# Performance work log

Measured on AMD Instinct MI355X. Metric: run time of the kernel, lower is better.

The kernel has to match this reference:

```python
import jax, jax.numpy as jnp
import numpy as np

NUM_GROUPS = 4
EPS = 1e-6


def group_norm(x, scale, bias):
    # x: [b, c, h, w]; GroupNorm32 computes stats in fp32 (x already fp32 here)
    b, c, h, w = x.shape
    xg = x.reshape(b, NUM_GROUPS, c // NUM_GROUPS, h, w)
    mean = jnp.mean(xg, axis=(2, 3, 4), keepdims=True)
    var = jnp.var(xg, axis=(2, 3, 4), keepdims=True)
    xn = ((xg - mean) * jax.lax.rsqrt(var + EPS)).reshape(b, c, h, w)
    return xn * scale[None, :, None, None] + bias[None, :, None, None]


def conv1x1(x, w, b):
    # 1x1 conv == channel mix: x [b,c,h,w], w [co,ci]
    return jnp.einsum('bchw,dc->bdhw', x, w) + b[None, :, None, None]


def setup_inputs() -> dict:
    key = jax.random.key(0)
    ks = jax.random.split(key, 6)
    c = 256
    s = 1.0 / np.sqrt(c)
    return {
        'x': jax.random.normal(ks[0], (4, c, 64, 64), dtype=jnp.float32),
        'gn_scale': jnp.ones((c,), jnp.float32),
        'gn_bias': jnp.zeros((c,), jnp.float32),
        'wq': jax.random.normal(ks[1], (c, c), jnp.float32) * s,
        'bq': jnp.zeros((c,), jnp.float32),
        'wk': jax.random.normal(ks[2], (c, c), jnp.float32) * s,
        'bk': jnp.zeros((c,), jnp.float32),
        'wv': jax.random.normal(ks[3], (c, c), jnp.float32) * s,
        'bv': jnp.zeros((c,), jnp.float32),
        'wproj': jax.random.normal(ks[4], (c, c), jnp.float32) * s,
        'bproj': jnp.zeros((c,), jnp.float32),
    }


def reference(x, gn_scale, gn_bias, wq, bq, wk, bk, wv, bv, wproj, bproj):
    b, c, h, w = x.shape
    hw = h * w
    h_ = group_norm(x, gn_scale, gn_bias)
    q = conv1x1(h_, wq, bq).reshape(b, c, hw)  # [b, c, hw]
    k = conv1x1(h_, wk, bk).reshape(b, c, hw)
    v = conv1x1(h_, wv, bv).reshape(b, c, hw)
    scale = jnp.float32(1.0 / np.sqrt(c))
    # attn[b, i, j] = sum_c q[b,c,i] * k[b,c,j], fp32 softmax over j
    attn = jnp.einsum('bci,bcj->bij', q.astype(jnp.float32), k.astype(jnp.float32)) * scale
    attn = jax.nn.softmax(attn, axis=-1).astype(x.dtype)
    # out[b, c, i] = sum_j v[b,c,j] * attn[b,i,j]
    out = jnp.einsum('bcj,bij->bci', v, attn).reshape(b, c, h, w)
    out = conv1x1(out, wproj, bproj)
    return x + out
```

## Files before the change

kernel.cpp:

```cpp
#include <hip/hip_runtime.h>


#define HW 4096
#define CCH 256
#define NBATCH 4
#define GN_N (64 * HW)

typedef unsigned short u16;
typedef __attribute__((ext_vector_type(8))) short bf16x8;
typedef __attribute__((ext_vector_type(4))) float f32x4;
typedef __attribute__((ext_vector_type(4))) u16 u16x4;

__device__ __forceinline__ u16 f2bf(float f) {
  unsigned u = __float_as_uint(f);
  u += 0x7fffu + ((u >> 16) & 1u);
  return (u16)(u >> 16);
}
__device__ __forceinline__ float bf2f(u16 h) { return __uint_as_float(((unsigned)h) << 16); }

__device__ __forceinline__ void gload_lds16(const void* g, void* l) {
  __builtin_amdgcn_global_load_lds(
      (const __attribute__((address_space(1))) unsigned*)g,
      (__attribute__((address_space(3))) unsigned*)l, 16, 0, 0);
}

__global__ __launch_bounds__(256) void gn_partial(const float* __restrict__ x,
                                                  float* __restrict__ part) {
  const int bg = blockIdx.y, blk = blockIdx.x, tid = threadIdx.x;
  const float4* X = (const float4*)(x + (size_t)bg * GN_N);
  float s = 0.f, ss = 0.f;
#pragma unroll
  for (int u = 0; u < 8; ++u) {
    float4 v = X[blk * 2048 + u * 256 + tid];
    s += v.x + v.y + v.z + v.w;
    ss += v.x * v.x + v.y * v.y + v.z * v.z + v.w * v.w;
  }
  for (int off = 32; off; off >>= 1) { s += __shfl_xor(s, off); ss += __shfl_xor(ss, off); }
  __shared__ float rs[4], rss[4];
  const int w = tid >> 6;
  if ((tid & 63) == 0) { rs[w] = s; rss[w] = ss; }
  __syncthreads();
  if (tid == 0) {
    part[(bg * 32 + blk) * 2 + 0] = rs[0] + rs[1] + rs[2] + rs[3];
    part[(bg * 32 + blk) * 2 + 1] = rss[0] + rss[1] + rss[2] + rss[3];
  }
}

__global__ void gn_finalize(const float* __restrict__ part, float2* __restrict__ stats) {
  const int t = threadIdx.x;
  if (t < 16) {
    float s = 0.f, ss = 0.f;
    for (int u = 0; u < 32; ++u) { s += part[(t * 32 + u) * 2]; ss += part[(t * 32 + u) * 2 + 1]; }
    const float mean = s * (1.0f / GN_N);
    const float var = ss * (1.0f / GN_N) - mean * mean;
    stats[t] = make_float2(mean, rsqrtf(var + 1e-6f));
  }
}

__global__ __launch_bounds__(256) void norm_tr(const float* __restrict__ x,
                                               const float2* __restrict__ stats,
                                               const float* __restrict__ gsc,
                                               const float* __restrict__ gbi,
                                               u16* __restrict__ Ht) {
  __shared__ u16 T[64][72];
  const int i0 = blockIdx.x * 64, c0 = blockIdx.y * 64, b = blockIdx.z;
  const int tid = threadIdx.x;
  const int cl = tid >> 4;
  const int il4 = (tid & 15) * 4;
#pragma unroll
  for (int it = 0; it < 4; ++it) {
    const int c = c0 + it * 16 + cl;
    const float2 st = stats[b * 4 + (c >> 6)];
    const float sc = gsc[c] * st.y;
    const float bi = gbi[c] - st.x * sc;
    const float4 v = *(const float4*)&x[((size_t)(b * CCH + c)) * HW + i0 + il4];
    T[il4 + 0][it * 16 + cl] = f2bf(v.x * sc + bi);
    T[il4 + 1][it * 16 + cl] = f2bf(v.y * sc + bi);
    T[il4 + 2][it * 16 + cl] = f2bf(v.z * sc + bi);
    T[il4 + 3][it * 16 + cl] = f2bf(v.w * sc + bi);
  }
  __syncthreads();
  const int il = tid >> 2, cs = (tid & 3) * 16;
  const uint4 a = *(const uint4*)&T[il][cs];
  const uint4 b2 = *(const uint4*)&T[il][cs + 8];
  const size_t o = ((size_t)b * HW + i0 + il) * CCH + c0 + cs;
  *(uint4*)&Ht[o] = a;
  *(uint4*)&Ht[o + 8] = b2;
}

__global__ __launch_bounds__(256) void wcast(const float* __restrict__ w0, const float* __restrict__ w1,
                                             const float* __restrict__ w2, const float* __restrict__ w3,
                                             u16* __restrict__ dst) {
  const float* src = blockIdx.y == 0 ? w0 : blockIdx.y == 1 ? w1 : blockIdx.y == 2 ? w2 : w3;
  u16* d = dst + (size_t)blockIdx.y * 65536;
  const int idx = (blockIdx.x * 256 + threadIdx.x) * 8;
  const float4 a = *(const float4*)&src[idx];
  const float4 c = *(const float4*)&src[idx + 4];
  uint4 p;
  p.x = (unsigned)f2bf(a.x) | ((unsigned)f2bf(a.y) << 16);
  p.y = (unsigned)f2bf(a.z) | ((unsigned)f2bf(a.w) << 16);
  p.z = (unsigned)f2bf(c.x) | ((unsigned)f2bf(c.y) << 16);
  p.w = (unsigned)f2bf(c.z) | ((unsigned)f2bf(c.w) << 16);
  *(uint4*)&d[idx] = p;
}

template <int EPI, bool HASB>
__global__ __launch_bounds__(256) void gemm2(
    const u16* __restrict__ A, int lda, long sA,
    const u16* __restrict__ Bm, int ldb, long sB,
    void* __restrict__ O0, int ldo, long sO,
    void* __restrict__ O1, void* __restrict__ O2,
    const float* __restrict__ b0, const float* __restrict__ b1, const float* __restrict__ b2,
    const float* __restrict__ aux, long sAux,
    float scale, int K) {
  __shared__ char lsA[32768], lsB[32768];
  int bx, by, bz;
  {
    const int nx = gridDim.x, ny = gridDim.y;
    const int lin = blockIdx.x + nx * (blockIdx.y + ny * blockIdx.z);
    const int q = (nx * ny * (int)gridDim.z) >> 3;
    const int wg = (lin & 7) * q + (lin >> 3);
    bx = wg % nx; const int t2 = wg / nx; by = t2 % ny; bz = t2 / ny;
  }
  const int tid = threadIdx.x;
  const int w = tid >> 6, l = tid & 63;
  const int wm = w >> 1, wn = w & 1;
  const int m0 = by * 128, n0 = bx * 128;
  const u16* Ab = A + (size_t)bz * sA;
  const u16* Bb = Bm + (size_t)bz * sB;

  f32x4 acc[4][4];
#pragma unroll
  for (int i = 0; i < 4; ++i)
#pragma unroll
    for (int j = 0; j < 4; ++j)
#pragma unroll
      for (int q2 = 0; q2 < 4; ++q2) acc[i][j][q2] = 0.f;

  auto stage = [&](int buf, int k0) {
#pragma unroll
    for (int s = 0; s < 4; ++s) {
      const int o = s * 4096 + tid * 16;
      const int r = o >> 7;
      const int c = ((o >> 4) & 7) ^ (r & 7);
      const int ke = c * 8;
      gload_lds16(Ab + (size_t)(m0 + r) * lda + k0 + ke, lsA + buf * 16384 + s * 4096 + w * 1024);
      gload_lds16(Bb + (size_t)(n0 + r) * ldb + k0 + ke, lsB + buf * 16384 + s * 4096 + w * 1024);
    }
  };

  const int nt = K >> 6;
  stage(0, 0);
  asm volatile("s_waitcnt vmcnt(0)" ::: "memory");
  __syncthreads();
  for (int t = 0; t < nt; ++t) {
    const int cur = t & 1;
    if (t + 1 < nt) stage(cur ^ 1, (t + 1) << 6);
#pragma unroll
    for (int kk = 0; kk < 2; ++kk) {
      bf16x8 aF[4], bF[4];
#pragma unroll
      for (int mi = 0; mi < 4; ++mi) {
        const int r = wm * 64 + mi * 16 + (l & 15);
        const int cc = (kk * 4 + (l >> 4)) ^ (r & 7);
        aF[mi] = *(const bf16x8*)(lsA + cur * 16384 + r * 128 + cc * 16);
      }
#pragma unroll
      for (int ni = 0; ni < 4; ++ni) {
        const int r = wn * 64 + ni * 16 + (l & 15);
        const int cc = (kk * 4 + (l >> 4)) ^ (r & 7);
        bF[ni] = *(const bf16x8*)(lsB + cur * 16384 + r * 128 + cc * 16);
      }
#pragma unroll
      for (int mi = 0; mi < 4; ++mi)
#pragma unroll
        for (int ni = 0; ni < 4; ++ni)
          acc[mi][ni] = __builtin_amdgcn_mfma_f32_16x16x32_bf16(aF[mi], bF[ni], acc[mi][ni], 0, 0, 0);
    }
    asm volatile("s_waitcnt vmcnt(0)" ::: "memory");
    __syncthreads();
  }

  const int lc = l & 15;
  const int lr4 = (l >> 4) * 4;

  if (EPI == 5) {
    const int sel = m0 >> 8;
    const float* bs = sel == 0 ? b0 : sel == 1 ? b1 : b2;
#pragma unroll
    for (int mi = 0; mi < 4; ++mi) {
      const int mg = m0 + wm * 64 + mi * 16 + lr4;
      const int mloc = mg & 255;
      const float4 bv = *(const float4*)&bs[mloc];
      float bb4[4] = {bv.x, bv.y, bv.z, bv.w};
#pragma unroll
      for (int ni = 0; ni < 4; ++ni) {
        const int n = n0 + wn * 64 + ni * 16 + lc;
        if (sel == 2) {
          u16* V = (u16*)O2 + (size_t)bz * sO;
#pragma unroll
          for (int q2 = 0; q2 < 4; ++q2) V[(size_t)(mloc + q2) * HW + n] = f2bf(acc[mi][ni][q2] + bb4[q2]);
        } else {
          u16* Oq = (u16*)(sel == 0 ? O0 : O1) + (size_t)bz * sO;
          u16x4 pk;
#pragma unroll
          for (int q2 = 0; q2 < 4; ++q2) pk[q2] = f2bf(acc[mi][ni][q2] + bb4[q2]);
          *(u16x4*)&Oq[(size_t)n * CCH + mloc] = pk;
        }
      }
    }
  } else {
    float* O = (float*)O0 + (size_t)bz * sO;
    const float* R = aux + (size_t)bz * sAux;
#pragma unroll
    for (int mi = 0; mi < 4; ++mi) {
      const int mb = m0 + wm * 64 + mi * 16 + lr4;
      float bb4[4] = {0.f, 0.f, 0.f, 0.f};
      if (HASB) {
        const float4 bv = *(const float4*)&b0[mb];
        bb4[0] = bv.x; bb4[1] = bv.y; bb4[2] = bv.z; bb4[3] = bv.w;
      }
#pragma unroll
      for (int ni = 0; ni < 4; ++ni) {
        const int n = n0 + wn * 64 + ni * 16 + lc;
#pragma unroll
        for (int q2 = 0; q2 < 4; ++q2)
          O[(size_t)(mb + q2) * ldo + n] = acc[mi][ni][q2] * scale + bb4[q2] + R[(size_t)(mb + q2) * ldo + n];
      }
    }
  }
}

#define LBUFA 32768
__global__ __launch_bounds__(256) void attn_fused(
    const u16* __restrict__ Qt, const u16* __restrict__ Kt, const u16* __restrict__ Vv,
    float* __restrict__ Opart, float* __restrict__ Rpart) {
  __shared__ __attribute__((aligned(16))) char lds[2 * LBUFA];
  __shared__ __attribute__((aligned(16))) unsigned P_block[64][20];
  const int bid = blockIdx.x;
  const int it = bid >> 3, b = (bid >> 1) & 3, jh = bid & 1;
  const int tid = threadIdx.x, w = tid >> 6, l = tid & 63;
  const int g = l >> 4, base = l & 15;
  const u16* Qb = Qt + (size_t)b * HW * CCH;
  const u16* Kb = Kt + (size_t)b * HW * CCH;
  const u16* Vb = Vv + (size_t)b * CCH * HW;
  const int iw0 = it * 64 + w * 16;

  bf16x8 q[8];
#pragma unroll
  for (int kc = 0; kc < 8; ++kc)
    q[kc] = *(const bf16x8*)&Qb[(size_t)(iw0 + base) * CCH + kc * 32 + g * 8];

  f32x4 oacc[4][4];
#pragma unroll
  for (int fi = 0; fi < 4; ++fi)
#pragma unroll
    for (int cf = 0; cf < 4; ++cf)
#pragma unroll
      for (int r = 0; r < 4; ++r) oacc[fi][cf][r] = 0.f;
  float rsum = 0.f;

  auto stage = [&](int buf, int j0) {
    char* Kl = lds + buf * LBUFA;
    char* Vl = Kl + 16384;
#pragma unroll
    for (int s = 0; s < 8; ++s) {
      const int i = s * 4 + w;
      if (i < 16) {
        const int row = i * 2 + (l >> 5);
        const int c5 = l & 31;
        gload_lds16(Kb + (size_t)(j0 + row) * CCH + ((c5 ^ (row & 7)) * 8), Kl + i * 1024);
      } else {
        const int jj = i - 16;
        const int jg = jj >> 2, sub = jj & 3;
        const int cc = sub * 64 + l;
        gload_lds16(Vb + (size_t)cc * HW + j0 + jg * 8, Vl + jg * 4096 + sub * 1024);
      }
    }
  };

  const int j0base = jh * 2048;
  const int NT = 64;
  stage(0, j0base);
  asm volatile("s_waitcnt vmcnt(0)" ::: "memory");
  __builtin_amdgcn_s_barrier();

  for (int t = 0; t < NT; ++t) {
    const int cur = t & 1;
    if (t + 1 < NT) stage(cur ^ 1, j0base + (t + 1) * 32);
    const char* Kl = lds + cur * LBUFA;
    const char* Vl = Kl + 16384;
    f32x4 sacc[2];
#pragma unroll
    for (int mj = 0; mj < 2; ++mj)
#pragma unroll
      for (int r = 0; r < 4; ++r) sacc[mj][r] = 0.f;
    __builtin_amdgcn_s_setprio(1);
#pragma unroll
    for (int kc = 0; kc < 8; ++kc) {
      bf16x8 kf[2];
#pragma unroll
      for (int mj = 0; mj < 2; ++mj) {
        const int row = mj * 16 + base;
        const int c5 = (kc * 4 + g) ^ (row & 7);
        kf[mj] = *(const bf16x8*)(Kl + row * 512 + c5 * 16);
      }
#pragma unroll
      for (int mj = 0; mj < 2; ++mj)
        sacc[mj] = __builtin_amdgcn_mfma_f32_16x16x32_bf16(kf[mj], q[kc], sacc[mj], 0, 0, 0);
    }
    __builtin_amdgcn_s_setprio(0);
    const int iL = w * 16 + base;
#pragma unroll
    for (int mj = 0; mj < 2; ++mj) {
      const float p0 = __expf(sacc[mj][0] * 0.0625f - 8.0f);
      const float p1 = __expf(sacc[mj][1] * 0.0625f - 8.0f);
      const float p2 = __expf(sacc[mj][2] * 0.0625f - 8.0f);
      const float p3 = __expf(sacc[mj][3] * 0.0625f - 8.0f);
      const u16 e0 = f2bf(p0), e1 = f2bf(p1), e2 = f2bf(p2), e3 = f2bf(p3);
      rsum += (bf2f(e0) + bf2f(e1)) + (bf2f(e2) + bf2f(e3));
      P_block[iL][mj * 8 + g * 2 + 0] = (unsigned)e0 | ((unsigned)e1 << 16);
      P_block[iL][mj * 8 + g * 2 + 1] = (unsigned)e2 | ((unsigned)e3 << 16);
    }
    asm volatile("s_waitcnt lgkmcnt(0)" ::: "memory");
    __builtin_amdgcn_sched_barrier(0);
    __builtin_amdgcn_s_barrier();
    bf16x8 vf[4];
#pragma unroll
    for (int cf = 0; cf < 4; ++cf)
      vf[cf] = *(const bf16x8*)(Vl + g * 4096 + (w * 64 + cf * 16 + base) * 16);
    __builtin_amdgcn_s_setprio(1);
#pragma unroll
    for (int fi = 0; fi < 4; ++fi) {
      const bf16x8 af = *(const bf16x8*)&P_block[fi * 16 + base][g * 4];
#pragma unroll
      for (int cf = 0; cf < 4; ++cf)
        oacc[fi][cf] = __builtin_amdgcn_mfma_f32_16x16x32_bf16(af, vf[cf], oacc[fi][cf], 0, 0, 0);
    }
    __builtin_amdgcn_s_setprio(0);
    asm volatile("s_waitcnt vmcnt(0) lgkmcnt(0)" ::: "memory");
    __builtin_amdgcn_sched_barrier(0);
    __builtin_amdgcn_s_barrier();
  }

  rsum += __shfl_xor(rsum, 16);
  rsum += __shfl_xor(rsum, 32);
  if (l < 16) Rpart[(size_t)jh * 16384 + b * HW + iw0 + l] = rsum;
  float* Op = Opart + (size_t)jh * 16384 * CCH + (size_t)b * HW * CCH + (size_t)it * 64 * CCH;
#pragma unroll
  for (int fi = 0; fi < 4; ++fi) {
#pragma unroll
    for (int cf = 0; cf < 4; ++cf) {
      const int c = w * 64 + cf * 16 + base;
#pragma unroll
      for (int r = 0; r < 4; ++r)
        Op[(size_t)(fi * 16 + g * 4 + r) * CCH + c] = oacc[fi][cf][r];
    }
  }
}

__global__ __launch_bounds__(256) void attn_combine(const float* __restrict__ Op,
                                                    const float* __restrict__ Rp,
                                                    u16* __restrict__ Ot) {
  const int idx = blockIdx.x * 256 + threadIdx.x;
  const int row = idx >> 6;
  const int c4 = (idx & 63) * 4;
  const float4 o0 = *(const float4*)&Op[(size_t)row * CCH + c4];
  const float4 o1 = *(const float4*)&Op[(size_t)16384 * CCH + (size_t)row * CCH + c4];
  const float inv = 1.0f / (Rp[row] + Rp[16384 + row]);
  u16x4 r;
  r[0] = f2bf((o0.x + o1.x) * inv);
  r[1] = f2bf((o0.y + o1.y) * inv);
  r[2] = f2bf((o0.z + o1.z) * inv);
  r[3] = f2bf((o0.w + o1.w) * inv);
  *(u16x4*)&Ot[(size_t)row * CCH + c4] = r;
}

extern "C" void kernel_launch(void* const* d_in, const int* in_sizes, int n_in,
                              void* d_out, int out_size, void* d_ws, size_t ws_size,
                              hipStream_t stream) {
  const float* x   = (const float*)d_in[0];
  const float* gsc = (const float*)d_in[1];
  const float* gbi = (const float*)d_in[2];
  const float* wq  = (const float*)d_in[3];
  const float* bq  = (const float*)d_in[4];
  const float* wk  = (const float*)d_in[5];
  const float* bk  = (const float*)d_in[6];
  const float* wv  = (const float*)d_in[7];
  const float* bv  = (const float*)d_in[8];
  const float* wp  = (const float*)d_in[9];
  const float* bp  = (const float*)d_in[10];
  float* out = (float*)d_out;

  char* ws = (char*)d_ws;
  size_t off = 0;
  auto alloc = [&](size_t bytes) {
    size_t o = off; off = (off + bytes + 255) & ~(size_t)255; return o;
  };
  const size_t szMat = (size_t)NBATCH * HW * CCH * 2;
  u16* W      = (u16*)(ws + alloc(4 * 65536 * 2));
  float* pgn  = (float*)(ws + alloc(16 * 32 * 2 * 4));
  float2* st  = (float2*)(ws + alloc(16 * 8));
  u16* Ht = (u16*)(ws + alloc(szMat));
  u16* Qt = (u16*)(ws + alloc(szMat));
  u16* Kt = (u16*)(ws + alloc(szMat));
  u16* Vv = (u16*)(ws + alloc(szMat));
  u16* Ot = (u16*)(ws + alloc(szMat));
  float* Opart = (float*)(ws + alloc((size_t)2 * 16384 * CCH * 4));
  float* Rpart = (float*)(ws + alloc((size_t)2 * 16384 * 4));

  const long sM = (long)HW * CCH;

  wcast<<<dim3(32, 4), 256, 0, stream>>>(wq, wk, wv, wp, W);
  gn_partial<<<dim3(32, 16), 256, 0, stream>>>(x, pgn);
  gn_finalize<<<1, 64, 0, stream>>>(pgn, st);
  norm_tr<<<dim3(HW / 64, CCH / 64, NBATCH), 256, 0, stream>>>(x, st, gsc, gbi, Ht);

  gemm2<5, true><<<dim3(32, 6, NBATCH), 256, 0, stream>>>(
      W, 256, 0, Ht, 256, sM, Qt, 256, sM, Kt, Vv, bq, bk, bv, nullptr, 0, 1.f, 256);

  attn_fused<<<512, 256, 0, stream>>>(Qt, Kt, Vv, Opart, Rpart);
  attn_combine<<<4096, 256, 0, stream>>>(Opart, Rpart, Ot);

  gemm2<2, true><<<dim3(32, 2, NBATCH), 256, 0, stream>>>(
      W + 3 * 65536, 256, 0, Ot, 256, sM, out, HW, (long)CCH * HW, nullptr, nullptr,
      bp, nullptr, nullptr, x, (long)CCH * HW, 1.f, 256);
}
```

Baseline: 187.7 us.

## Switch attention to 32x32x16 MFMA with 64-key tiles and blocked V layout

Rewrites the fused attention kernel to use 32x32x16 bf16 MFMA instead of 16x16x32. Each block now stages 64 keys per iteration, giving half as many loop trips and barriers, and each wave computes a 32x32 score tile. The V projection epilogue now writes an 8-column blocked layout so V tiles load contiguously. Row sums are split across two key halves per block, so the combine kernel sums four partials. LDS use doubles to 128KB plus a larger P buffer, which limits occupancy to one block per CU.

New measurement: 188.6 us. Within noise of the previous version (+0.5%).

```diff
diff --git a/kernel.cpp b/kernel.cpp
--- a/kernel.cpp
+++ b/kernel.cpp
@@ -9,6 +9,7 @@
 typedef unsigned short u16;
 typedef __attribute__((ext_vector_type(8))) short bf16x8;
 typedef __attribute__((ext_vector_type(4))) float f32x4;
+typedef __attribute__((ext_vector_type(16))) float f32x16;
 typedef __attribute__((ext_vector_type(4))) u16 u16x4;
 
 __device__ __forceinline__ u16 f2bf(float f) {
@@ -198,8 +199,10 @@
         const int n = n0 + wn * 64 + ni * 16 + lc;
         if (sel == 2) {
           u16* V = (u16*)O2 + (size_t)bz * sO;
-#pragma unroll
-          for (int q2 = 0; q2 < 4; ++q2) V[(size_t)(mloc + q2) * HW + n] = f2bf(acc[mi][ni][q2] + bb4[q2]);
+          const size_t vb = (size_t)(n >> 3) * 2048 + (n & 7);
+#pragma unroll
+          for (int q2 = 0; q2 < 4; ++q2)
+            V[vb + (size_t)(mloc + q2) * 8] = f2bf(acc[mi][ni][q2] + bb4[q2]);
         } else {
           u16* Oq = (u16*)(sel == 0 ? O0 : O1) + (size_t)bz * sO;
           u16x4 pk;
@@ -231,111 +234,112 @@
   }
 }
 
-#define LBUFA 32768
 __global__ __launch_bounds__(256) void attn_fused(
-    const u16* __restrict__ Qt, const u16* __restrict__ Kt, const u16* __restrict__ Vv,
+    const u16* __restrict__ Qt, const u16* __restrict__ Kt, const u16* __restrict__ Vg,
     float* __restrict__ Opart, float* __restrict__ Rpart) {
-  __shared__ __attribute__((aligned(16))) char lds[2 * LBUFA];
-  __shared__ __attribute__((aligned(16))) unsigned P_block[64][20];
+  __shared__ __attribute__((aligned(16))) char lds[2][65536];
+  __shared__ __attribute__((aligned(16))) unsigned P_block[64][36];
   const int bid = blockIdx.x;
   const int it = bid >> 3, b = (bid >> 1) & 3, jh = bid & 1;
   const int tid = threadIdx.x, w = tid >> 6, l = tid & 63;
-  const int g = l >> 4, base = l & 15;
+  const int l31 = l & 31, h5 = l >> 5;
+  const int jb = w >> 1, ib = w & 1;
   const u16* Qb = Qt + (size_t)b * HW * CCH;
   const u16* Kb = Kt + (size_t)b * HW * CCH;
-  const u16* Vb = Vv + (size_t)b * CCH * HW;
-  const int iw0 = it * 64 + w * 16;
-
-  bf16x8 q[8];
-#pragma unroll
-  for (int kc = 0; kc < 8; ++kc)
-    q[kc] = *(const bf16x8*)&Qb[(size_t)(iw0 + base) * CCH + kc * 32 + g * 8];
-
-  f32x4 oacc[4][4];
-#pragma unroll
-  for (int fi = 0; fi < 4; ++fi)
-#pragma unroll
-    for (int cf = 0; cf < 4; ++cf)
-#pragma unroll
-      for (int r = 0; r < 4; ++r) oacc[fi][cf][r] = 0.f;
+  const u16* Vb = Vg + (size_t)b * HW * CCH;
+  const int iw0 = it * 64;
+
+  bf16x8 q[16];
+#pragma unroll
+  for (int kc = 0; kc < 16; ++kc)
+    q[kc] = *(const bf16x8*)&Qb[(size_t)(iw0 + ib * 32 + l31) * CCH + kc * 16 + h5 * 8];
+
+  f32x16 oacc[2][2];
+#pragma unroll
+  for (int i = 0; i < 2; ++i)
+#pragma unroll
+    for (int j = 0; j < 2; ++j)
+#pragma unroll
+      for (int r = 0; r < 16; ++r) oacc[i][j][r] = 0.f;
   float rsum = 0.f;
 
   auto stage = [&](int buf, int j0) {
-    char* Kl = lds + buf * LBUFA;
-    char* Vl = Kl + 16384;
-#pragma unroll
-    for (int s = 0; s < 8; ++s) {
+    char* Kl = lds[buf];
+    char* Vl = Kl + 32768;
+#pragma unroll
+    for (int s = 0; s < 16; ++s) {
       const int i = s * 4 + w;
-      if (i < 16) {
+      if (i < 32) {
         const int row = i * 2 + (l >> 5);
         const int c5 = l & 31;
         gload_lds16(Kb + (size_t)(j0 + row) * CCH + ((c5 ^ (row & 7)) * 8), Kl + i * 1024);
       } else {
-        const int jj = i - 16;
+        const int jj = i - 32;
         const int jg = jj >> 2, sub = jj & 3;
         const int cc = sub * 64 + l;
-        gload_lds16(Vb + (size_t)cc * HW + j0 + jg * 8, Vl + jg * 4096 + sub * 1024);
+        gload_lds16(Vb + (size_t)((j0 >> 3) + jg) * 2048 + cc * 8, Vl + jg * 4096 + sub * 1024);
       }
     }
   };
 
   const int j0base = jh * 2048;
-  const int NT = 64;
+  const int NT = 32;
   stage(0, j0base);
   asm volatile("s_waitcnt vmcnt(0)" ::: "memory");
   __builtin_amdgcn_s_barrier();
 
   for (int t = 0; t < NT; ++t) {
     const int cur = t & 1;
-    if (t + 1 < NT) stage(cur ^ 1, j0base + (t + 1) * 32);
-    const char* Kl = lds + cur * LBUFA;
-    const char* Vl = Kl + 16384;
-    f32x4 sacc[2];
-#pragma unroll
-    for (int mj = 0; mj < 2; ++mj)
-#pragma unroll
-      for (int r = 0; r < 4; ++r) sacc[mj][r] = 0.f;
+    if (t + 1 < NT) stage(cur ^ 1, j0base + (t + 1) * 64);
+    const char* Kl = lds[cur];
+    const char* Vl = Kl + 32768;
+    f32x16 sacc;
+#pragma unroll
+    for (int r = 0; r < 16; ++r) sacc[r] = 0.f;
     __builtin_amdgcn_s_setprio(1);
 #pragma unroll
-    for (int kc = 0; kc < 8; ++kc) {
-      bf16x8 kf[2];
-#pragma unroll
-      for (int mj = 0; mj < 2; ++mj) {
-        const int row = mj * 16 + base;
-        const int c5 = (kc * 4 + g) ^ (row & 7);
-        kf[mj] = *(const bf16x8*)(Kl + row * 512 + c5 * 16);
-      }
-#pragma unroll
-      for (int mj = 0; mj < 2; ++mj)
-        sacc[mj] = __builtin_amdgcn_mfma_f32_16x16x32_bf16(kf[mj], q[kc], sacc[mj], 0, 0, 0);
+    for (int kc = 0; kc < 16; ++kc) {
+      const int row = jb * 32 + l31;
+      const int c5 = (kc * 2 + h5) ^ (row & 7);
+      const bf16x8 kf = *(const bf16x8*)(Kl + row * 512 + c5 * 16);
+      sacc = __builtin_amdgcn_mfma_f32_32x32x16_bf16(kf, q[kc], sacc, 0, 0, 0);
     }
     __builtin_amdgcn_s_setprio(0);
-    const int iL = w * 16 + base;
-#pragma unroll
-    for (int mj = 0; mj < 2; ++mj) {
-      const float p0 = __expf(sacc[mj][0] * 0.0625f - 8.0f);
-      const float p1 = __expf(sacc[mj][1] * 0.0625f - 8.0f);
-      const float p2 = __expf(sacc[mj][2] * 0.0625f - 8.0f);
-      const float p3 = __expf(sacc[mj][3] * 0.0625f - 8.0f);
-      const u16 e0 = f2bf(p0), e1 = f2bf(p1), e2 = f2bf(p2), e3 = f2bf(p3);
-      rsum += (bf2f(e0) + bf2f(e1)) + (bf2f(e2) + bf2f(e3));
-      P_block[iL][mj * 8 + g * 2 + 0] = (unsigned)e0 | ((unsigned)e1 << 16);
-      P_block[iL][mj * 8 + g * 2 + 1] = (unsigned)e2 | ((unsigned)e3 << 16);
+    {
+      const int iL = ib * 32 + l31;
+#pragma unroll
+      for (int a = 0; a < 4; ++a) {
+        const float p0 = __expf(sacc[4 * a + 0] * 0.0625f - 8.0f);
+        const float p1 = __expf(sacc[4 * a + 1] * 0.0625f - 8.0f);
+        const float p2 = __expf(sacc[4 * a + 2] * 0.0625f - 8.0f);
+        const float p3 = __expf(sacc[4 * a + 3] * 0.0625f - 8.0f);
+        const u16 e0 = f2bf(p0), e1 = f2bf(p1), e2 = f2bf(p2), e3 = f2bf(p3);
+        rsum += (bf2f(e0) + bf2f(e1)) + (bf2f(e2) + bf2f(e3));
+        *(uint2*)&P_block[iL][jb * 16 + 4 * a + 2 * h5] =
+            make_uint2((unsigned)e0 | ((unsigned)e1 << 16),
+                       (unsigned)e2 | ((unsigned)e3 << 16));
+      }
     }
     asm volatile("s_waitcnt lgkmcnt(0)" ::: "memory");
     __builtin_amdgcn_sched_barrier(0);
     __builtin_amdgcn_s_barrier();
-    bf16x8 vf[4];
-#pragma unroll
-    for (int cf = 0; cf < 4; ++cf)
-      vf[cf] = *(const bf16x8*)(Vl + g * 4096 + (w * 64 + cf * 16 + base) * 16);
     __builtin_amdgcn_s_setprio(1);
 #pragma unroll
-    for (int fi = 0; fi < 4; ++fi) {
-      const bf16x8 af = *(const bf16x8*)&P_block[fi * 16 + base][g * 4];
-#pragma unroll
-      for (int cf = 0; cf < 4; ++cf)
-        oacc[fi][cf] = __builtin_amdgcn_mfma_f32_16x16x32_bf16(af, vf[cf], oacc[fi][cf], 0, 0, 0);
+    for (int js16 = 0; js16 < 4; ++js16) {
+      bf16x8 af[2], vf[2];
+#pragma unroll
+      for (int itile = 0; itile < 2; ++itile)
+        af[itile] = *(const bf16x8*)&P_block[itile * 32 + l31][js16 * 8 + h5 * 4];
+#pragma unroll
+      for (int ct = 0; ct < 2; ++ct) {
+        const int c = w * 64 + ct * 32 + l31;
+        vf[ct] = *(const bf16x8*)(Vl + (js16 * 2 + h5) * 4096 + c * 16);
+      }
+#pragma unroll
+      for (int itile = 0; itile < 2; ++itile)
+#pragma unroll
+        for (int ct = 0; ct < 2; ++ct)
+          oacc[itile][ct] = __builtin_amdgcn_mfma_f32_32x32x16_bf16(af[itile], vf[ct], oacc[itile][ct], 0, 0, 0);
     }
     __builtin_amdgcn_s_setprio(0);
     asm volatile("s_waitcnt vmcnt(0) lgkmcnt(0)" ::: "memory");
@@ -343,20 +347,21 @@
     __builtin_amdgcn_s_barrier();
   }
 
-  rsum += __shfl_xor(rsum, 16);
   rsum += __shfl_xor(rsum, 32);
-  if (l < 16) Rpart[(size_t)jh * 16384 + b * HW + iw0 + l] = rsum;
-  float* Op = Opart + (size_t)jh * 16384 * CCH + (size_t)b * HW * CCH + (size_t)it * 64 * CCH;
-#pragma unroll
-  for (int fi = 0; fi < 4; ++fi) {
-#pragma unroll
-    for (int cf = 0; cf < 4; ++cf) {
-      const int c = w * 64 + cf * 16 + base;
-#pragma unroll
-      for (int r = 0; r < 4; ++r)
-        Op[(size_t)(fi * 16 + g * 4 + r) * CCH + c] = oacc[fi][cf][r];
-    }
-  }
+  if (l < 32)
+    Rpart[(size_t)(jh * 2 + jb) * 16384 + b * HW + iw0 + ib * 32 + l31] = rsum;
+  float* Op = Opart + (size_t)jh * 16384 * CCH + (size_t)b * HW * CCH + (size_t)iw0 * CCH;
+#pragma unroll
+  for (int itile = 0; itile < 2; ++itile)
+#pragma unroll
+    for (int ct = 0; ct < 2; ++ct) {
+      const int c = w * 64 + ct * 32 + l31;
+#pragma unroll
+      for (int r = 0; r < 16; ++r) {
+        const int row = itile * 32 + (r & 3) + 8 * (r >> 2) + 4 * h5;
+        Op[(size_t)row * CCH + c] = oacc[itile][ct][r];
+      }
+    }
 }
 
 __global__ __launch_bounds__(256) void attn_combine(const float* __restrict__ Op,
@@ -367,7 +372,10 @@
   const int c4 = (idx & 63) * 4;
   const float4 o0 = *(const float4*)&Op[(size_t)row * CCH + c4];
   const float4 o1 = *(const float4*)&Op[(size_t)16384 * CCH + (size_t)row * CCH + c4];
-  const float inv = 1.0f / (Rp[row] + Rp[16384 + row]);
+  float rs = 0.f;
+#pragma unroll
+  for (int s = 0; s < 4; ++s) rs += Rp[(size_t)s * 16384 + row];
+  const float inv = 1.0f / rs;
   u16x4 r;
   r[0] = f2bf((o0.x + o1.x) * inv);
   r[1] = f2bf((o0.y + o1.y) * inv);
@@ -404,10 +412,10 @@
   u16* Ht = (u16*)(ws + alloc(szMat));
   u16* Qt = (u16*)(ws + alloc(szMat));
   u16* Kt = (u16*)(ws + alloc(szMat));
-  u16* Vv = (u16*)(ws + alloc(szMat));
+  u16* Vg = (u16*)(ws + alloc(szMat));
   u16* Ot = (u16*)(ws + alloc(szMat));
   float* Opart = (float*)(ws + alloc((size_t)2 * 16384 * CCH * 4));
-  float* Rpart = (float*)(ws + alloc((size_t)2 * 16384 * 4));
+  float* Rpart = (float*)(ws + alloc((size_t)4 * 16384 * 4));
 
   const long sM = (long)HW * CCH;
 
@@ -417,9 +425,9 @@
   norm_tr<<<dim3(HW / 64, CCH / 64, NBATCH), 256, 0, stream>>>(x, st, gsc, gbi, Ht);
 
   gemm2<5, true><<<dim3(32, 6, NBATCH), 256, 0, stream>>>(
-      W, 256, 0, Ht, 256, sM, Qt, 256, sM, Kt, Vv, bq, bk, bv, nullptr, 0, 1.f, 256);
-
-  attn_fused<<<512, 256, 0, stream>>>(Qt, Kt, Vv, Opart, Rpart);
+      W, 256, 0, Ht, 256, sM, Qt, 256, sM, Kt, Vg, bq, bk, bv, nullptr, 0, 1.f, 256);
+
+  attn_fused<<<512, 256, 0, stream>>>(Qt, Kt, Vg, Opart, Rpart);
   attn_combine<<<4096, 256, 0, stream>>>(Opart, Rpart, Ot);
 
   gemm2<2, true><<<dim3(32, 2, NBATCH), 256, 0, stream>>>(
```
